# Kernel tuning notes

Hardware: AMD Instinct MI355X
Metric: run time of the kernel (lower is better)

Reference implementation:

```python
import jax, jax.numpy as jnp
import numpy as np

KS = (5, 5, 5)      # dilated_kernel_size (Kd, Kh, Kw)
STRIDE = (1, 1, 1)
PADDING = (2, 2, 2)
GROUPS = 1


def construct_kernel(W, P, ks):
    # W: (oc, ic/g, kc), P: (3, oc, ic/g, kc)
    Kd, Kh, Kw = ks
    lim = jnp.floor_divide(jnp.array([Kd, Kh, Kw], dtype=P.dtype), 2.0)
    Pp = P + lim[:, None, None, None]          # shift to grid coords
    Pf = jnp.floor(Pp)
    R = Pp - Pf                                # fractional parts, (3, oc, ic, kc)
    P1, P2, P3 = Pf[0], Pf[1], Pf[2]
    R1, R2, R3 = R[0], R[1], R[2]
    # trilinear weights factorize per axis. In the torch original:
    #   L (depth axis, Kd)  compares against P1/R1
    #   I (width axis, Kw)  compares against P2/R2
    #   J (height axis, Kh) compares against P3/R3
    gL = jnp.arange(Kd, dtype=P.dtype)[:, None, None, None]
    gJ = jnp.arange(Kh, dtype=P.dtype)[:, None, None, None]
    gI = jnp.arange(Kw, dtype=P.dtype)[:, None, None, None]
    aL = (gL == P1) * (1.0 - R1) + (gL == P1 + 1.0) * R1   # (Kd, oc, ic, kc)
    aJ = (gJ == P3) * (1.0 - R3) + (gJ == P3 + 1.0) * R3   # (Kh, oc, ic, kc)
    aI = (gI == P2) * (1.0 - R2) + (gI == P2 + 1.0) * R2   # (Kw, oc, ic, kc)
    # K[o,c,l,j,i] = sum_k W[o,c,k] * aL[l,o,c,k] * aJ[j,o,c,k] * aI[i,o,c,k]
    K = jnp.einsum('ock,lock,jock,iock->oclji', W, aL, aJ, aI)
    return K  # (oc, ic/g, Kd, Kh, Kw)


def setup_inputs() -> dict:
    key = jax.random.key(0)
    k1, k2, k3, k4 = jax.random.split(key, 4)
    x = jax.random.normal(k1, (2, 32, 16, 32, 32), dtype=jnp.float32)
    weight = jax.random.normal(k2, (64, 32, 16), dtype=jnp.float32) * 0.05
    P = jax.random.normal(k3, (3, 64, 32, 16), dtype=jnp.float32) * 0.5
    bias = jax.random.normal(k4, (64,), dtype=jnp.float32) * 0.05
    return {"x": x, "weight": weight, "P": P, "bias": bias}


def reference(x, weight, P, bias):
    K = construct_kernel(weight, P, KS)
    out = jax.lax.conv_general_dilated(
        x, K,
        window_strides=STRIDE,
        padding=[(p, p) for p in PADDING],
        dimension_numbers=('NCDHW', 'OIDHW', 'NCDHW'),
        feature_group_count=GROUPS,
    )
    return out + bias[None, :, None, None, None]
```

## Files before the change

### kernel.cpp

```cpp
#include <hip/hip_runtime.h>

#define OC 64
#define IC 32
#define KC 16

typedef __attribute__((ext_vector_type(8))) short bf16x8;
typedef __attribute__((ext_vector_type(16))) float f32x16;

__device__ inline unsigned short f2bf(float f) {
    unsigned u = __builtin_bit_cast(unsigned, f);
    unsigned r = (u + 0x7fffu + ((u >> 16) & 1u)) >> 16;
    return (unsigned short)r;
}

__global__ __launch_bounds__(128) void prep(const float* __restrict__ x,
                                            const float* __restrict__ W,
                                            const float* __restrict__ P,
                                            short* __restrict__ xp,
                                            short* __restrict__ Kb) {
    const int b = blockIdx.x;
    if (b < 1440) {
        const int n = b / 720;
        const int rem = b - n * 720;
        const int z = rem / 36;
        const int h = rem - z * 36;
        const int zr = z - 2, hr = h - 2;
        short* orow = xp + (size_t)((n * 20 + z) * 36 + h) * 1152;

        if ((unsigned)zr >= 16u || (unsigned)hr >= 32u) {
            for (int idx = threadIdx.x; idx < 144; idx += 128)
                *reinterpret_cast<float4*>(orow + idx * 8) =
                    make_float4(0.f, 0.f, 0.f, 0.f);
            return;
        }

        __shared__ float sR[32][36];
        const float* xb = x + ((size_t)(n * 32) * 16 + zr) * 1024 + hr * 32;
        for (int idx = threadIdx.x; idx < 32 * 36; idx += 128) {
            const int c = idx / 36;
            const int w = idx - c * 36;
            const int wr = w - 2;
            float v = 0.f;
            if ((unsigned)wr < 32u) v = xb[(size_t)c * 16384 + wr];
            sR[c][w] = v;
        }
        __syncthreads();
        for (int idx = threadIdx.x; idx < 144; idx += 128) {
            const int cg = idx / 36;
            const int w  = idx - cg * 36;
            bf16x8 pk;
            #pragma unroll
            for (int e = 0; e < 8; ++e) pk[e] = (short)f2bf(sR[cg * 8 + e][w]);
            *reinterpret_cast<bf16x8*>(orow + idx * 8) = pk;
        }
    } else {
        const int pair = b - 1440;
        const int o = pair >> 5;
        const int c = pair & 31;
        const int cell = threadIdx.x;
        if (cell >= 125) return;
        const int l = cell / 25;
        const int j = (cell / 5) % 5;
        const int i = cell % 5;
        const float fl = (float)l, fj = (float)j, fi = (float)i;
        const int base = (o * IC + c) * KC;
        float acc = 0.f;
        #pragma unroll
        for (int k = 0; k < KC; ++k) {
            const float w  = W[base + k];
            const float p1 = P[0 * OC * IC * KC + base + k] + 2.0f;
            const float p2 = P[1 * OC * IC * KC + base + k] + 2.0f;
            const float p3 = P[2 * OC * IC * KC + base + k] + 2.0f;
            const float f1 = floorf(p1), r1 = p1 - f1;
            const float f2 = floorf(p2), r2 = p2 - f2;
            const float f3 = floorf(p3), r3 = p3 - f3;
            const float wl = (fl == f1) ? (1.f - r1) : ((fl == f1 + 1.f) ? r1 : 0.f);
            const float wj = (fj == f3) ? (1.f - r3) : ((fj == f3 + 1.f) ? r3 : 0.f);
            const float wi = (fi == f2) ? (1.f - r2) : ((fi == f2 + 1.f) ? r2 : 0.f);
            acc += w * (wl * wj * wi);
        }
        const int og = o >> 5;
        Kb[(size_t)(og * 125 + cell) * 1024 + (c >> 3) * 256 + (o & 31) * 8 + (c & 7)] =
            (short)f2bf(acc);
    }
}

#define ASLOT 25600
#define BBASE 51200
#define BSLOT 13824

__global__ __launch_bounds__(256, 1) void conv_mfma(const short* __restrict__ Kb,
                                                    const short* __restrict__ xp,
                                                    const float* __restrict__ bias,
                                                    float* __restrict__ out) {
    const int sw = (blockIdx.x & 7) * 32 + (blockIdx.x >> 3);
    const int og = sw & 1;
    const int hb = (sw >> 1) & 3;
    const int d  = (sw >> 3) & 15;
    const int n  = sw >> 7;
    const int h0 = hb * 8;

    __shared__ short sL[2 * ASLOT + 2 * BSLOT];

    const int tid  = threadIdx.x;
    const int wv   = tid >> 6;
    const int lane = tid & 63;
    const int wcol = lane & 31;
    const int hi   = lane >> 5;

    const short* srcA0 = Kb + (size_t)(og * 125) * 1024;
    const short* srcB0 = xp + ((size_t)(n * 20 + d) * 36 + h0) * 1152;

    const int aoff = wcol * 8 + hi * 256;
    const int boff = hi * 288 + wcol * 8;

    f32x16 acc0, acc1;
    for (int e = 0; e < 16; ++e) { acc0[e] = 0.f; acc1[e] = 0.f; }

    bf16x8 Ab[3][2];
    bf16x8 Aq[3][2][5];
    bf16x8 Bq[3][2][5];

#define STAGEA(L, BUF)                                                        \
    {                                                                         \
        const short* s_ = srcA0 + (size_t)(L) * 25600;                        \
        short* d_ = sL + (BUF) * ASLOT;                                       \
        _Pragma("unroll")                                                     \
        for (int k_ = 0; k_ < 12; ++k_) {                                     \
            const int t_ = k_ * 256 + tid;                                    \
            __builtin_amdgcn_global_load_lds(                                 \
                (const __attribute__((address_space(1))) unsigned int*)(s_ + t_ * 8), \
                (__attribute__((address_space(3))) unsigned int*)(d_ + t_ * 8), \
                16, 0, 0);                                                    \
        }                                                                     \
        if (tid < 128) {                                                      \
            const int t_ = 3072 + tid;                                        \
            __builtin_amdgcn_global_load_lds(                                 \
                (const __attribute__((address_space(1))) unsigned int*)(s_ + t_ * 8), \
                (__attribute__((address_space(3))) unsigned int*)(d_ + t_ * 8), \
                16, 0, 0);                                                    \
        }                                                                     \
    }

#define STAGEB(L, BUF)                                                        \
    {                                                                         \
        const short* s_ = srcB0 + (size_t)(L) * 41472;                        \
        short* d_ = sL + BBASE + (BUF) * BSLOT;                               \
        _Pragma("unroll")                                                     \
        for (int k_ = 0; k_ < 6; ++k_) {                                      \
            const int t_ = k_ * 256 + tid;                                    \
            __builtin_amdgcn_global_load_lds(                                 \
                (const __attribute__((address_space(1))) unsigned int*)(s_ + t_ * 8), \
                (__attribute__((address_space(3))) unsigned int*)(d_ + t_ * 8), \
                16, 0, 0);                                                    \
        }                                                                     \
        if (tid < 192) {                                                      \
            const int t_ = 1536 + tid;                                        \
            __builtin_amdgcn_global_load_lds(                                 \
                (const __attribute__((address_space(1))) unsigned int*)(s_ + t_ * 8), \
                (__attribute__((address_space(3))) unsigned int*)(d_ + t_ * 8), \
                16, 0, 0);                                                    \
        }                                                                     \
    }

#define LOADA(S, BUF, J)                                                      \
    {                                                                         \
        const short* pa_ = sL + (BUF) * ASLOT + (J) * 5120 + aoff;            \
        _Pragma("unroll")                                                     \
        for (int i_ = 0; i_ < 5; ++i_) {                                      \
            Aq[S][0][i_] = *reinterpret_cast<const bf16x8*>(pa_ + i_ * 1024); \
            Aq[S][1][i_] = *reinterpret_cast<const bf16x8*>(pa_ + i_ * 1024 + 512); \
        }                                                                     \
    }

#define LOADB(S, BUF, K)                                                      \
    {                                                                         \
        const short* pb_ = sL + BBASE + (BUF) * BSLOT + (2 * wv + (K)) * 1152 + boff; \
        _Pragma("unroll")                                                     \
        for (int i_ = 0; i_ < 5; ++i_) {                                      \
            Bq[S][0][i_] = *reinterpret_cast<const bf16x8*>(pb_ + i_ * 8);    \
            Bq[S][1][i_] = *reinterpret_cast<const bf16x8*>(pb_ + 576 + i_ * 8); \
        }                                                                     \
    }

#define MFMA_STEP(RA, S0, S1)                                                 \
    {                                                                         \
        __builtin_amdgcn_s_setprio(1);                                        \
        _Pragma("unroll")                                                     \
        for (int i_ = 0; i_ < 5; ++i_) {                                      \
            acc0 = __builtin_amdgcn_mfma_f32_32x32x16_bf16(Aq[RA][0][i_], Bq[S0][0][i_], acc0, 0, 0, 0); \
            acc1 = __builtin_amdgcn_mfma_f32_32x32x16_bf16(Aq[RA][0][i_], Bq[S1][0][i_], acc1, 0, 0, 0); \
            acc0 = __builtin_amdgcn_mfma_f32_32x32x16_bf16(Aq[RA][1][i_], Bq[S0][1][i_], acc0, 0, 0, 0); \
            acc1 = __builtin_amdgcn_mfma_f32_32x32x16_bf16(Aq[RA][1][i_], Bq[S1][1][i_], acc1, 0, 0, 0); \
        }                                                                     \
        __builtin_amdgcn_s_setprio(0);                                        \
    }

    STAGEA(0, 0);
    STAGEB(0, 0);
    __syncthreads();

    #pragma unroll
    for (int l = 0; l < 5; ++l) {
        const int buf = l & 1;
        if (l < 4) { STAGEA(l + 1, buf ^ 1); STAGEB(l + 1, buf ^ 1); }
        LOADA(0, buf, 0); LOADA(1, buf, 1);
        LOADB(0, buf, 0); LOADB(1, buf, 1);
        #pragma unroll
        for (int j = 0; j < 5; ++j) {
            if (j < 3) LOADA((j + 2) % 3, buf, j + 2);
            if (j < 4) LOADB((j + 2) % 3, buf, j + 2);
            MFMA_STEP(j % 3, j % 3, (j + 1) % 3);
        }
        if (l < 4) __syncthreads();
    }

#undef STAGEA
#undef STAGEB
#undef LOADA
#undef LOADB
#undef MFMA_STEP

    const int h = h0 + 2 * wv;
    #pragma unroll
    for (int reg = 0; reg < 16; ++reg) {
        const int o = og * 32 + (reg & 3) + 8 * (reg >> 2) + 4 * hi;
        const float bo = bias[o];
        float* op = out + (((size_t)(n * 64 + o) * 16 + d) * 32 + h) * 32 + wcol;
        op[0]  = acc0[reg] + bo;
        op[32] = acc1[reg] + bo;
    }
}

extern "C" void kernel_launch(void* const* d_in, const int* in_sizes, int n_in,
                              void* d_out, int out_size, void* d_ws, size_t ws_size,
                              hipStream_t stream) {
    const float* x    = (const float*)d_in[0];
    const float* W    = (const float*)d_in[1];
    const float* P    = (const float*)d_in[2];
    const float* bias = (const float*)d_in[3];
    float* outp = (float*)d_out;

    short* Kb = (short*)d_ws;
    short* xp = (short*)((char*)d_ws + 524288);

    prep<<<1440 + 2048, 128, 0, stream>>>(x, W, P, xp, Kb);
    conv_mfma<<<256, 256, 0, stream>>>(Kb, xp, bias, outp);
}
```

Before: 28.64 us.

## Split reduction over channel halves across 8 waves with LDS partial-sum combine

Doubles the conv block from 4 to 8 waves. Each pair of waves splits the 32-input-channel K dimension into two halves, so each wave issues half as many MFMAs and holds half as many A/B fragments. The partial accumulators are combined through LDS before the bias add and the store. The goal is more latency hiding and MFMA parallelism per CU. The cost is an extra reduction pass through shared memory and two more block-wide barriers.

Result: faster. 27.02 us (-5.7%).

```diff
diff --git a/kernel.cpp b/kernel.cpp
--- a/kernel.cpp
+++ b/kernel.cpp
@@ -89,7 +89,7 @@
 #define BBASE 51200
 #define BSLOT 13824
 
-__global__ __launch_bounds__(256, 1) void conv_mfma(const short* __restrict__ Kb,
+__global__ __launch_bounds__(512, 1) void conv_mfma(const short* __restrict__ Kb,
                                                     const short* __restrict__ xp,
                                                     const float* __restrict__ bias,
                                                     float* __restrict__ out) {
@@ -104,6 +104,8 @@
 
     const int tid  = threadIdx.x;
     const int wv   = tid >> 6;
+    const int hp   = wv >> 1;
+    const int g    = wv & 1;
     const int lane = tid & 63;
     const int wcol = lane & 31;
     const int hi   = lane >> 5;
@@ -111,23 +113,22 @@
     const short* srcA0 = Kb + (size_t)(og * 125) * 1024;
     const short* srcB0 = xp + ((size_t)(n * 20 + d) * 36 + h0) * 1152;
 
-    const int aoff = wcol * 8 + hi * 256;
-    const int boff = hi * 288 + wcol * 8;
+    const int aoff = wcol * 8 + (g * 2 + hi) * 256;
+    const int boff = (g * 2 + hi) * 288 + wcol * 8;
 
     f32x16 acc0, acc1;
     for (int e = 0; e < 16; ++e) { acc0[e] = 0.f; acc1[e] = 0.f; }
 
-    bf16x8 Ab[3][2];
-    bf16x8 Aq[3][2][5];
-    bf16x8 Bq[3][2][5];
+    bf16x8 Aq[3][5];
+    bf16x8 Bq[3][5];
 
 #define STAGEA(L, BUF)                                                        \
     {                                                                         \
         const short* s_ = srcA0 + (size_t)(L) * 25600;                        \
         short* d_ = sL + (BUF) * ASLOT;                                       \
         _Pragma("unroll")                                                     \
-        for (int k_ = 0; k_ < 12; ++k_) {                                     \
-            const int t_ = k_ * 256 + tid;                                    \
+        for (int k_ = 0; k_ < 6; ++k_) {                                      \
+            const int t_ = k_ * 512 + tid;                                    \
             __builtin_amdgcn_global_load_lds(                                 \
                 (const __attribute__((address_space(1))) unsigned int*)(s_ + t_ * 8), \
                 (__attribute__((address_space(3))) unsigned int*)(d_ + t_ * 8), \
@@ -147,8 +148,8 @@
         const short* s_ = srcB0 + (size_t)(L) * 41472;                        \
         short* d_ = sL + BBASE + (BUF) * BSLOT;                               \
         _Pragma("unroll")                                                     \
-        for (int k_ = 0; k_ < 6; ++k_) {                                      \
-            const int t_ = k_ * 256 + tid;                                    \
+        for (int k_ = 0; k_ < 3; ++k_) {                                      \
+            const int t_ = k_ * 512 + tid;                                    \
             __builtin_amdgcn_global_load_lds(                                 \
                 (const __attribute__((address_space(1))) unsigned int*)(s_ + t_ * 8), \
                 (__attribute__((address_space(3))) unsigned int*)(d_ + t_ * 8), \
@@ -167,31 +168,25 @@
     {                                                                         \
         const short* pa_ = sL + (BUF) * ASLOT + (J) * 5120 + aoff;            \
         _Pragma("unroll")                                                     \
+        for (int i_ = 0; i_ < 5; ++i_)                                        \
+            Aq[S][i_] = *reinterpret_cast<const bf16x8*>(pa_ + i_ * 1024);    \
+    }
+
+#define LOADB(S, BUF, K)                                                      \
+    {                                                                         \
+        const short* pb_ = sL + BBASE + (BUF) * BSLOT + (2 * hp + (K)) * 1152 + boff; \
+        _Pragma("unroll")                                                     \
+        for (int i_ = 0; i_ < 5; ++i_)                                        \
+            Bq[S][i_] = *reinterpret_cast<const bf16x8*>(pb_ + i_ * 8);       \
+    }
+
+#define MFMA_STEP(RA, S0, S1)                                                 \
+    {                                                                         \
+        __builtin_amdgcn_s_setprio(1);                                        \
+        _Pragma("unroll")                                                     \
         for (int i_ = 0; i_ < 5; ++i_) {                                      \
-            Aq[S][0][i_] = *reinterpret_cast<const bf16x8*>(pa_ + i_ * 1024); \
-            Aq[S][1][i_] = *reinterpret_cast<const bf16x8*>(pa_ + i_ * 1024 + 512); \
-        }                                                                     \
-    }
-
-#define LOADB(S, BUF, K)                                                      \
-    {                                                                         \
-        const short* pb_ = sL + BBASE + (BUF) * BSLOT + (2 * wv + (K)) * 1152 + boff; \
-        _Pragma("unroll")                                                     \
-        for (int i_ = 0; i_ < 5; ++i_) {                                      \
-            Bq[S][0][i_] = *reinterpret_cast<const bf16x8*>(pb_ + i_ * 8);    \
-            Bq[S][1][i_] = *reinterpret_cast<const bf16x8*>(pb_ + 576 + i_ * 8); \
-        }                                                                     \
-    }
-
-#define MFMA_STEP(RA, S0, S1)                                                 \
-    {                                                                         \
-        __builtin_amdgcn_s_setprio(1);                                        \
-        _Pragma("unroll")                                                     \
-        for (int i_ = 0; i_ < 5; ++i_) {                                      \
-            acc0 = __builtin_amdgcn_mfma_f32_32x32x16_bf16(Aq[RA][0][i_], Bq[S0][0][i_], acc0, 0, 0, 0); \
-            acc1 = __builtin_amdgcn_mfma_f32_32x32x16_bf16(Aq[RA][0][i_], Bq[S1][0][i_], acc1, 0, 0, 0); \
-            acc0 = __builtin_amdgcn_mfma_f32_32x32x16_bf16(Aq[RA][1][i_], Bq[S0][1][i_], acc0, 0, 0, 0); \
-            acc1 = __builtin_amdgcn_mfma_f32_32x32x16_bf16(Aq[RA][1][i_], Bq[S1][1][i_], acc1, 0, 0, 0); \
+            acc0 = __builtin_amdgcn_mfma_f32_32x32x16_bf16(Aq[RA][i_], Bq[S0][i_], acc0, 0, 0, 0); \
+            acc1 = __builtin_amdgcn_mfma_f32_32x32x16_bf16(Aq[RA][i_], Bq[S1][i_], acc1, 0, 0, 0); \
         }                                                                     \
         __builtin_amdgcn_s_setprio(0);                                        \
     }
@@ -221,14 +216,26 @@
 #undef LOADB
 #undef MFMA_STEP
 
-    const int h = h0 + 2 * wv;
-    #pragma unroll
-    for (int reg = 0; reg < 16; ++reg) {
-        const int o = og * 32 + (reg & 3) + 8 * (reg >> 2) + 4 * hi;
-        const float bo = bias[o];
-        float* op = out + (((size_t)(n * 64 + o) * 16 + d) * 32 + h) * 32 + wcol;
-        op[0]  = acc0[reg] + bo;
-        op[32] = acc1[reg] + bo;
+    __syncthreads();
+    float* sF = reinterpret_cast<float*>(sL);
+    if (g == 1) {
+        #pragma unroll
+        for (int e = 0; e < 16; ++e) {
+            sF[hp * 2048 + e * 64 + lane]        = acc0[e];
+            sF[hp * 2048 + (e + 16) * 64 + lane] = acc1[e];
+        }
+    }
+    __syncthreads();
+    if (g == 0) {
+        const int h = h0 + 2 * hp;
+        #pragma unroll
+        for (int reg = 0; reg < 16; ++reg) {
+            const int o = og * 32 + (reg & 3) + 8 * (reg >> 2) + 4 * hi;
+            const float bo = bias[o];
+            float* op = out + (((size_t)(n * 64 + o) * 16 + d) * 32 + h) * 32 + wcol;
+            op[0]  = acc0[reg] + sF[hp * 2048 + reg * 64 + lane] + bo;
+            op[32] = acc1[reg] + sF[hp * 2048 + (reg + 16) * 64 + lane] + bo;
+        }
     }
 }
 
@@ -245,5 +252,5 @@
     short* xp = (short*)((char*)d_ws + 524288);
 
     prep<<<1440 + 2048, 128, 0, stream>>>(x, W, P, xp, Kb);
-    conv_mfma<<<256, 256, 0, stream>>>(Kb, xp, bias, outp);
-}
+    conv_mfma<<<256, 512, 0, stream>>>(Kb, xp, bias, outp);
+}
```
